# Performance work log

Hardware: AMD Instinct MI355X
Metric: run time of the kernel (lower is better)

## Reference

```python
import jax, jax.numpy as jnp
import numpy as np

BITS = 4
ELEMS_PER_BYTE = 8 // BITS  # 2
BLOCK_SIZE = 128
IN_FEATURES = 8192
OUT_FEATURES = 28672
BATCH = 8


def _make_lut():
    # lut1 = linspace(-1, 1, 2**bits); lut = cartesian_prod(lut1, lut1) -> [256, 2]
    lut1 = jnp.linspace(-1.0, 1.0, 2 ** BITS, dtype=jnp.float32)
    a, b = jnp.meshgrid(lut1, lut1, indexing="ij")
    return jnp.stack([a.reshape(-1), b.reshape(-1)], axis=-1)  # [256, 2]


def setup_inputs() -> dict:
    key = jax.random.key(0)
    k1, k2, k3 = jax.random.split(key, 3)
    x = jax.random.normal(k1, (BATCH, IN_FEATURES), dtype=jnp.float32)
    weight_data = jax.random.randint(
        k2, (OUT_FEATURES, IN_FEATURES // ELEMS_PER_BYTE), 0, 256, dtype=jnp.int32
    )
    # per-(out, block) absmax scale, strictly positive
    scale = jax.random.uniform(
        k3, (OUT_FEATURES, IN_FEATURES // BLOCK_SIZE), dtype=jnp.float32,
        minval=0.01, maxval=0.1,
    )
    lut = _make_lut()
    return {"x": x, "weight_data": weight_data, "scale": scale, "lut": lut}


def reference(x, weight_data, scale, lut):
    # LUT dequantisation: each packed byte indexes a [256, 2] table of value pairs.
    O = weight_data.shape[0]
    vals = lut[weight_data]                       # [O, I/2, 2]
    w = vals.reshape(O, -1)                       # [O, I] dequantised (unit-scale)
    n_blocks = scale.shape[1]
    w = (w.reshape(O, n_blocks, BLOCK_SIZE) * scale[:, :, None]).reshape(O, -1)
    # out[n, o] = sum_i x[n, i] * w[o, i]
    return jnp.einsum("ni,oi->no", x, w)
```

## Files before the change

kernel.cpp:

```cpp
#include <hip/hip_runtime.h>


#define O_TOTAL 28672
#define I_TOTAL 8192
#define QROW    4096
#define NBATCH  8
#define NBLK    64
#define CHUNK_I 1024
#define CHUNK_Q 512
#define NCHUNK  8

__global__ __launch_bounds__(256)
void qlinear_kernel(const float* __restrict__ x,
                    const int*   __restrict__ wq,
                    const float* __restrict__ scale,
                    float*       __restrict__ out) {
    __shared__ float xs[NBATCH][CHUNK_I];

    const int tid  = threadIdx.x;
    const int wave = tid >> 6;
    const int lane = tid & 63;
    const int o0   = blockIdx.x * 32 + wave * 8;

    float acc[64];
    #pragma unroll
    for (int i = 0; i < 64; ++i) acc[i] = 0.0f;

    for (int c = 0; c < NCHUNK; ++c) {
        __syncthreads();
        #pragma unroll
        for (int n = 0; n < NBATCH; ++n) {
            *(float4*)&xs[n][tid * 4] =
                *(const float4*)&x[n * I_TOTAL + c * CHUNK_I + tid * 4];
        }
        __syncthreads();

        #pragma unroll
        for (int j2 = 0; j2 < 8; ++j2) {
            const int q = c * CHUNK_Q + j2 * 64 + lane;

            int wraw[8];
            #pragma unroll
            for (int r = 0; r < 8; ++r)
                wraw[r] = wq[(size_t)(o0 + r) * QROW + q];

            float sc[8];
            #pragma unroll
            for (int r = 0; r < 8; ++r)
                sc[r] = scale[(o0 + r) * NBLK + c * 8 + j2];

            float xv[16];
            const int li = j2 * 128 + 2 * lane;
            #pragma unroll
            for (int n = 0; n < 8; ++n) {
                float2 t = *(const float2*)&xs[n][li];
                xv[2 * n]     = t.x;
                xv[2 * n + 1] = t.y;
            }

            #pragma unroll
            for (int r = 0; r < 8; ++r) {
                const float s   = sc[r];
                const float s2  = s * (2.0f / 15.0f);
                const float whi = fmaf((float)((wraw[r] >> 4) & 15), s2, -s);
                const float wlo = fmaf((float)( wraw[r]       & 15), s2, -s);
                #pragma unroll
                for (int n = 0; n < 8; ++n) {
                    acc[r * 8 + n] = fmaf(whi, xv[2 * n],
                                     fmaf(wlo, xv[2 * n + 1], acc[r * 8 + n]));
                }
            }
        }
    }

    float a[64];
    #pragma unroll
    for (int v = 0; v < 64; ++v) a[v] = acc[v];

    #pragma unroll
    for (int b = 0; b < 6; ++b) {
        const int keep = (lane >> b) & 1;
        const int m = 64 >> (b + 1);
        #pragma unroll
        for (int i = 0; i < m; ++i) {
            float lo   = a[2 * i];
            float hi   = a[2 * i + 1];
            float mine = keep ? hi : lo;
            float send = keep ? lo : hi;
            float t    = __shfl_xor(send, 1 << b, 64);
            a[i] = mine + t;
        }
    }

    const int r = lane >> 3;
    const int n = lane & 7;
    out[n * O_TOTAL + (o0 + r)] = a[0];
}

extern "C" void kernel_launch(void* const* d_in, const int* in_sizes, int n_in,
                              void* d_out, int out_size, void* d_ws, size_t ws_size,
                              hipStream_t stream) {
    const float* x     = (const float*)d_in[0];
    const int*   wq    = (const int*)  d_in[1];
    const float* scale = (const float*)d_in[2];
    float* out = (float*)d_out;

    dim3 grid(O_TOTAL / 32);
    dim3 block(256);
    qlinear_kernel<<<grid, block, 0, stream>>>(x, wq, scale, out);
}
```

Baseline: 682.4 us.

## Drop LDS staging, vectorize weight loads, and prefetch next weight tile

Removes the shared-memory staging of x and the block-wide barriers, so each lane reads x directly from global/L2 as float4. Each wave now handles 4 output rows instead of 8 and loads two packed ints per lane as int2, software-prefetching the next iteration's weights. The grid doubles and register pressure drops, which should raise occupancy and memory-level parallelism for this bandwidth-bound GEMV. The cost is redundant x reads across waves through the cache, plus a final cross-half shuffle in the reduction.

```diff
diff --git a/kernel.cpp b/kernel.cpp
--- a/kernel.cpp
+++ b/kernel.cpp
@@ -4,97 +4,93 @@
 #define O_TOTAL 28672
 #define I_TOTAL 8192
 #define QROW    4096
-#define NBATCH  8
 #define NBLK    64
-#define CHUNK_I 1024
-#define CHUNK_Q 512
-#define NCHUNK  8
+#define NITER   32
 
 __global__ __launch_bounds__(256)
 void qlinear_kernel(const float* __restrict__ x,
                     const int*   __restrict__ wq,
                     const float* __restrict__ scale,
                     float*       __restrict__ out) {
-    __shared__ float xs[NBATCH][CHUNK_I];
-
     const int tid  = threadIdx.x;
     const int wave = tid >> 6;
     const int lane = tid & 63;
-    const int o0   = blockIdx.x * 32 + wave * 8;
+    const int o0   = blockIdx.x * 16 + wave * 4;
 
-    float acc[64];
+    const int* wbase = wq + (size_t)o0 * QROW + 2 * lane;
+    const int  half  = lane >> 5;
+
+    float acc[32];
     #pragma unroll
-    for (int i = 0; i < 64; ++i) acc[i] = 0.0f;
+    for (int i = 0; i < 32; ++i) acc[i] = 0.0f;
 
-    for (int c = 0; c < NCHUNK; ++c) {
-        __syncthreads();
+    int2 wcur[4];
+    #pragma unroll
+    for (int r = 0; r < 4; ++r)
+        wcur[r] = *(const int2*)(wbase + r * QROW);
+
+    for (int j = 0; j < NITER; ++j) {
+        const int jn = (j + 1) & (NITER - 1);
+        int2 wnxt[4];
         #pragma unroll
-        for (int n = 0; n < NBATCH; ++n) {
-            *(float4*)&xs[n][tid * 4] =
-                *(const float4*)&x[n * I_TOTAL + c * CHUNK_I + tid * 4];
-        }
-        __syncthreads();
+        for (int r = 0; r < 4; ++r)
+            wnxt[r] = *(const int2*)(wbase + r * QROW + 128 * jn);
+
+        const int c0 = 256 * j + 4 * lane;
+        float4 xv[8];
+        #pragma unroll
+        for (int n = 0; n < 8; ++n)
+            xv[n] = *(const float4*)(x + n * I_TOTAL + c0);
+
+        const int b = 2 * j + half;
+        float sc[4];
+        #pragma unroll
+        for (int r = 0; r < 4; ++r)
+            sc[r] = scale[(o0 + r) * NBLK + b];
 
         #pragma unroll
-        for (int j2 = 0; j2 < 8; ++j2) {
-            const int q = c * CHUNK_Q + j2 * 64 + lane;
-
-            int wraw[8];
-            #pragma unroll
-            for (int r = 0; r < 8; ++r)
-                wraw[r] = wq[(size_t)(o0 + r) * QROW + q];
-
-            float sc[8];
-            #pragma unroll
-            for (int r = 0; r < 8; ++r)
-                sc[r] = scale[(o0 + r) * NBLK + c * 8 + j2];
-
-            float xv[16];
-            const int li = j2 * 128 + 2 * lane;
+        for (int r = 0; r < 4; ++r) {
+            const float s   = sc[r];
+            const float s2  = s * (2.0f / 15.0f);
+            const int   w01 = wcur[r].x;
+            const int   w23 = wcur[r].y;
+            const float wA  = fmaf((float)((w01 >> 4) & 15), s2, -s);
+            const float wB  = fmaf((float)( w01       & 15), s2, -s);
+            const float wC  = fmaf((float)((w23 >> 4) & 15), s2, -s);
+            const float wD  = fmaf((float)( w23       & 15), s2, -s);
             #pragma unroll
             for (int n = 0; n < 8; ++n) {
-                float2 t = *(const float2*)&xs[n][li];
-                xv[2 * n]     = t.x;
-                xv[2 * n + 1] = t.y;
-            }
-
-            #pragma unroll
-            for (int r = 0; r < 8; ++r) {
-                const float s   = sc[r];
-                const float s2  = s * (2.0f / 15.0f);
-                const float whi = fmaf((float)((wraw[r] >> 4) & 15), s2, -s);
-                const float wlo = fmaf((float)( wraw[r]       & 15), s2, -s);
-                #pragma unroll
-                for (int n = 0; n < 8; ++n) {
-                    acc[r * 8 + n] = fmaf(whi, xv[2 * n],
-                                     fmaf(wlo, xv[2 * n + 1], acc[r * 8 + n]));
-                }
+                float t = fmaf(wA, xv[n].x, acc[r * 8 + n]);
+                t       = fmaf(wB, xv[n].y, t);
+                t       = fmaf(wC, xv[n].z, t);
+                acc[r * 8 + n] = fmaf(wD, xv[n].w, t);
             }
         }
+
+        #pragma unroll
+        for (int r = 0; r < 4; ++r) wcur[r] = wnxt[r];
     }
 
-    float a[64];
     #pragma unroll
-    for (int v = 0; v < 64; ++v) a[v] = acc[v];
-
-    #pragma unroll
-    for (int b = 0; b < 6; ++b) {
-        const int keep = (lane >> b) & 1;
-        const int m = 64 >> (b + 1);
+    for (int bs = 0; bs < 5; ++bs) {
+        const int keep = (lane >> bs) & 1;
+        const int m = 32 >> (bs + 1);
         #pragma unroll
         for (int i = 0; i < m; ++i) {
-            float lo   = a[2 * i];
-            float hi   = a[2 * i + 1];
+            float lo   = acc[2 * i];
+            float hi   = acc[2 * i + 1];
             float mine = keep ? hi : lo;
             float send = keep ? lo : hi;
-            float t    = __shfl_xor(send, 1 << b, 64);
-            a[i] = mine + t;
+            acc[i] = mine + __shfl_xor(send, 1 << bs, 64);
         }
     }
+    float v = acc[0] + __shfl_xor(acc[0], 32, 64);
 
-    const int r = lane >> 3;
-    const int n = lane & 7;
-    out[n * O_TOTAL + (o0 + r)] = a[0];
+    if (lane < 32) {
+        const int r = lane >> 3;
+        const int n = lane & 7;
+        out[n * O_TOTAL + o0 + r] = v;
+    }
 }
 
 extern "C" void kernel_launch(void* const* d_in, const int* in_sizes, int n_in,
@@ -105,7 +101,7 @@
     const float* scale = (const float*)d_in[2];
     float* out = (float*)d_out;
 
-    dim3 grid(O_TOTAL / 32);
+    dim3 grid(O_TOTAL / 16);
     dim3 block(256);
     qlinear_kernel<<<grid, block, 0, stream>>>(x, wq, scale, out);
 }
```

Result: faster. 645.9 us (-5.4%).
